# Kernel optimization log

Measured on AMD Instinct MI355X. Metric: run time of the kernel, lower is better.

Reference implementation:

```python
import jax, jax.numpy as jnp
import numpy as np

NUM_HEADS = 8
WINDOW_SIZE = 4
DIM = 384


def setup_inputs() -> dict:
    key = jax.random.key(0)
    k_x, k_qkv, k_pw, k_pb = jax.random.split(key, 4)
    B, N, C = 8, 16384, DIM
    x = jax.random.normal(k_x, (B, N, C), dtype=jnp.float32)
    # torch nn.Linear weights are [out_features, in_features]
    W_qkv = jax.random.normal(k_qkv, (3 * C, C), dtype=jnp.float32) * (1.0 / np.sqrt(C))
    W_proj = jax.random.normal(k_pw, (C, C), dtype=jnp.float32) * (1.0 / np.sqrt(C))
    b_proj = jax.random.normal(k_pb, (C,), dtype=jnp.float32) * 0.01
    return {"x": x, "W_qkv": W_qkv, "W_proj": W_proj, "b_proj": b_proj}


def reference(x, W_qkv, W_proj, b_proj):
    B, N, C = x.shape
    H = int(round(N ** 0.5))
    W = H
    ws = WINDOW_SIZE
    nh = NUM_HEADS
    hd = C // nh
    scale = hd ** -0.5
    hw, ww = H // ws, W // ws

    qkv = x @ W_qkv.T  # [B, N, 3C]
    qkv = qkv.reshape(B, N, 3, nh, hd)
    qkv = jnp.transpose(qkv, (2, 0, 3, 1, 4))  # [3, B, nh, N, hd]
    q, k, v = qkv[0], qkv[1], qkv[2]

    def to_windows(t):
        # [B, nh, N, hd] -> [B, nh, n_windows, ws*ws, hd]
        t = t.reshape(B, nh, hw, ws, ww, ws, hd)
        t = jnp.transpose(t, (0, 1, 2, 4, 3, 5, 6))
        return t.reshape(B, nh, hw * ww, ws * ws, hd)

    q, k, v = to_windows(q), to_windows(k), to_windows(v)

    attn = jnp.einsum('bhwqd,bhwkd->bhwqk', q, k) * scale
    attn = jax.nn.softmax(attn, axis=-1)
    out = jnp.einsum('bhwqk,bhwkd->bhwqd', attn, v)

    # windows back to [B, N, C]
    out = out.reshape(B, nh, hw, ww, ws, ws, hd)
    out = jnp.transpose(out, (0, 1, 2, 4, 3, 5, 6)).reshape(B, nh, N, hd)
    out = jnp.transpose(out, (0, 2, 1, 3)).reshape(B, N, C)

    out = out @ W_proj.T + b_proj
    return out
```

## Files before the change

### kernel.cpp

```cpp
#include <hip/hip_runtime.h>
#include <hip/hip_bf16.h>
#include <cstdint>

#define ASPACE(n) __attribute__((address_space(n)))

typedef short bf16x8 __attribute__((ext_vector_type(8)));
typedef float f32x4 __attribute__((ext_vector_type(4)));

__device__ __forceinline__ unsigned short f2bf(float f) {
  uint32_t u = __float_as_uint(f);
  u += 0x7fffu + ((u >> 16) & 1u);
  return (unsigned short)(u >> 16);
}
__device__ __forceinline__ float bf2f(unsigned short h) {
  return __uint_as_float(((uint32_t)h) << 16);
}

__global__ __launch_bounds__(256) void conv_f32_bf16(const float4* __restrict__ src,
                                                     ushort4* __restrict__ dst, int n4) {
  int i = blockIdx.x * blockDim.x + threadIdx.x;
  int stride = gridDim.x * blockDim.x;
  for (; i < n4; i += stride) {
    float4 v = src[i];
    ushort4 o;
    o.x = f2bf(v.x); o.y = f2bf(v.y); o.z = f2bf(v.z); o.w = f2bf(v.w);
    dst[i] = o;
  }
}


__device__ __forceinline__ void gload16(const unsigned short* g, unsigned short* l) {
  __builtin_amdgcn_global_load_lds((const ASPACE(1) void*)g, (ASPACE(3) void*)l, 16, 0, 0);
}

template <int OUT_MODE>
__global__ __launch_bounds__(256, 3) void gemm_bt(const unsigned short* __restrict__ A,
                                                  const unsigned short* __restrict__ B,
                                                  void* __restrict__ Cout,
                                                  const float* __restrict__ bias,
                                                  int M, int N, int K) {
  __shared__ unsigned short As[2][128 * 32];
  __shared__ unsigned short Bs[2][192 * 32];

  const int tid  = threadIdx.x;
  const int lane = tid & 63;
  const int wave = tid >> 6;
  const int wr = wave >> 1;
  const int wc = wave & 1;

  const int nwg = gridDim.x;
  const int swz = (blockIdx.x & 7) * (nwg >> 3) + (blockIdx.x >> 3);
  const int ntn = N / 192;
  const int bn0 = (swz % ntn) * 192;
  const int bm0 = (swz / ntn) << 7;

  const unsigned short* Abase = A + (size_t)bm0 * K;
  const unsigned short* Bbase = B + (size_t)bn0 * K;

  const unsigned short* gA[2];
  const unsigned short* gB[3];
  unsigned short* lA[2];
  unsigned short* lB[3];
#pragma unroll
  for (int i = 0; i < 2; ++i) {
    const int c = i * 256 + tid;
    const int r = c >> 2;
    const int gc = (c & 3) ^ ((r >> 1) & 3);
    gA[i] = Abase + (size_t)r * K + gc * 8;
    lA[i] = (unsigned short*)As + (i * 256 + wave * 64) * 8;
  }
#pragma unroll
  for (int i = 0; i < 3; ++i) {
    const int c = i * 256 + tid;
    const int r = c >> 2;
    const int gc = (c & 3) ^ ((r >> 1) & 3);
    gB[i] = Bbase + (size_t)r * K + gc * 8;
    lB[i] = (unsigned short*)Bs + (i * 256 + wave * 64) * 8;
  }
  const int abufoff = 128 * 32;
  const int bbufoff = 192 * 32;

  const int fr = lane & 15;
  const int hi = lane >> 4;
  int afo[4], bfo[6];
#pragma unroll
  for (int m = 0; m < 4; ++m) {
    const int row = wr * 64 + m * 16 + fr;
    afo[m] = row * 32 + ((hi ^ ((row >> 1) & 3)) * 8);
  }
#pragma unroll
  for (int n = 0; n < 6; ++n) {
    const int row = wc * 96 + n * 16 + fr;
    bfo[n] = row * 32 + ((hi ^ ((row >> 1) & 3)) * 8);
  }

  f32x4 acc[4][6];
#pragma unroll
  for (int m = 0; m < 4; ++m)
#pragma unroll
    for (int n = 0; n < 6; ++n) {
      f32x4 z = {0.f, 0.f, 0.f, 0.f};
      acc[m][n] = z;
    }

  const int NT = K >> 5;

#pragma unroll
  for (int i = 0; i < 2; ++i) gload16(gA[i], lA[i]);
#pragma unroll
  for (int i = 0; i < 3; ++i) gload16(gB[i], lB[i]);
  __syncthreads();

  int cur = 0;
  for (int t = 0; t < NT; ++t) {
    if (t + 1 < NT) {
      const int nb = cur ^ 1;
      const int k0 = (t + 1) << 5;
#pragma unroll
      for (int i = 0; i < 2; ++i) gload16(gA[i] + k0, lA[i] + nb * abufoff);
#pragma unroll
      for (int i = 0; i < 3; ++i) gload16(gB[i] + k0, lB[i] + nb * bbufoff);
    }
    {
      const unsigned short* Ab = (const unsigned short*)As + cur * abufoff;
      const unsigned short* Bb = (const unsigned short*)Bs + cur * bbufoff;
      bf16x8 af[4], bfv[6];
#pragma unroll
      for (int m = 0; m < 4; ++m) af[m] = *(const bf16x8*)(Ab + afo[m]);
#pragma unroll
      for (int n = 0; n < 6; ++n) bfv[n] = *(const bf16x8*)(Bb + bfo[n]);
#pragma unroll
      for (int m = 0; m < 4; ++m)
#pragma unroll
        for (int n = 0; n < 6; ++n)
          acc[m][n] = __builtin_amdgcn_mfma_f32_16x16x32_bf16(af[m], bfv[n], acc[m][n], 0, 0, 0);
    }
    __syncthreads();
    cur ^= 1;
  }

  const int rq = hi * 4;
  if (OUT_MODE == 1) {
    float* C = (float*)Cout;
#pragma unroll
    for (int m = 0; m < 4; ++m) {
#pragma unroll
      for (int n = 0; n < 6; ++n) {
        const int col = bn0 + wc * 96 + n * 16 + fr;
        const float bv = bias[col];
#pragma unroll
        for (int r = 0; r < 4; ++r) {
          const int row = bm0 + wr * 64 + m * 16 + rq + r;
          C[(size_t)row * N + col] = acc[m][n][r] + bv;
        }
      }
    }
  } else {
    unsigned short* C = (unsigned short*)Cout;
#pragma unroll
    for (int m = 0; m < 4; ++m) {
#pragma unroll
      for (int n = 0; n < 6; ++n) {
        const int col = bn0 + wc * 96 + n * 16 + fr;
#pragma unroll
        for (int r = 0; r < 4; ++r) {
          const int row = bm0 + wr * 64 + m * 16 + rq + r;
          C[(size_t)row * N + col] = f2bf(acc[m][n][r]);
        }
      }
    }
  }
}

#define PADV 24
#define PADP 24
__global__ __launch_bounds__(256) void win_attn(const unsigned short* __restrict__ qkv,
                                                unsigned short* __restrict__ aout) {
  __shared__ unsigned short lds[4][48 * PADV + 16 * PADP];
  const int tid = threadIdx.x;
  const int wave = tid >> 6, lane = tid & 63;
  const int wg = blockIdx.x * 4 + wave;
  const int h = wg & 7;
  const int bw = wg >> 3;
  const int w = bw & 1023, b = bw >> 10;
  const int wy = w >> 5, wx = w & 31;

  unsigned short* Vt = lds[wave];
  unsigned short* P  = lds[wave] + 48 * PADV;

  const int lg = lane >> 4;
  const int lr = lane & 15;

  const int n_lr = (wy * 4 + (lr >> 2)) * 128 + wx * 4 + (lr & 3);
  const size_t rowbase = ((size_t)(b * 16384 + n_lr)) * 1152 + h * 48;

  bf16x8 aq0, bk0;
  bf16x8 aq1 = {0, 0, 0, 0, 0, 0, 0, 0};
  bf16x8 bk1 = {0, 0, 0, 0, 0, 0, 0, 0};
  aq0 = *(const bf16x8*)(qkv + rowbase + lg * 8);
  bk0 = *(const bf16x8*)(qkv + rowbase + 384 + lg * 8);
  if (lg < 2) {
    aq1 = *(const bf16x8*)(qkv + rowbase + 32 + lg * 8);
    bk1 = *(const bf16x8*)(qkv + rowbase + 384 + 32 + lg * 8);
  }

  {
    bf16x8 v = *(const bf16x8*)(qkv + rowbase + 768 + lg * 8);
#pragma unroll
    for (int i = 0; i < 8; ++i) Vt[(lg * 8 + i) * PADV + lr] = (unsigned short)v[i];
    if (lane < 32) {
      bf16x8 v2 = *(const bf16x8*)(qkv + rowbase + 768 + 32 + lg * 8);
#pragma unroll
      for (int i = 0; i < 8; ++i) Vt[((4 + lg) * 8 + i) * PADV + lr] = (unsigned short)v2[i];
    }
  }

  f32x4 s = {0.f, 0.f, 0.f, 0.f};
  s = __builtin_amdgcn_mfma_f32_16x16x32_bf16(aq0, bk0, s, 0, 0, 0);
  s = __builtin_amdgcn_mfma_f32_16x16x32_bf16(aq1, bk1, s, 0, 0, 0);

  const float scale = 0.14433756729740643f;
  float p[4];
#pragma unroll
  for (int r = 0; r < 4; ++r) {
    float x = s[r] * scale;
    float m = x;
    m = fmaxf(m, __shfl_xor(m, 1));
    m = fmaxf(m, __shfl_xor(m, 2));
    m = fmaxf(m, __shfl_xor(m, 4));
    m = fmaxf(m, __shfl_xor(m, 8));
    float e = __expf(x - m);
    float t = e;
    t += __shfl_xor(t, 1);
    t += __shfl_xor(t, 2);
    t += __shfl_xor(t, 4);
    t += __shfl_xor(t, 8);
    p[r] = e / t;
  }
#pragma unroll
  for (int r = 0; r < 4; ++r) P[(lg * 4 + r) * PADP + lr] = f2bf(p[r]);

  __syncthreads();

  bf16x8 ap = {0, 0, 0, 0, 0, 0, 0, 0};
  if (lg < 2) ap = *(const bf16x8*)(P + lr * PADP + lg * 8);

  f32x4 o[3];
#pragma unroll
  for (int c = 0; c < 3; ++c) {
    bf16x8 bv = {0, 0, 0, 0, 0, 0, 0, 0};
    if (lg < 2) bv = *(const bf16x8*)(Vt + (c * 16 + lr) * PADV + lg * 8);
    f32x4 z = {0.f, 0.f, 0.f, 0.f};
    o[c] = __builtin_amdgcn_mfma_f32_16x16x32_bf16(ap, bv, z, 0, 0, 0);
  }

#pragma unroll
  for (int r = 0; r < 4; ++r) {
    const int qi = lg * 4 + r;
    const int nq = (wy * 4 + (qi >> 2)) * 128 + wx * 4 + (qi & 3);
    const size_t obase = ((size_t)(b * 16384 + nq)) * 384 + h * 48;
#pragma unroll
    for (int c = 0; c < 3; ++c)
      aout[obase + c * 16 + lr] = f2bf(o[c][r]);
  }
}

extern "C" void kernel_launch(void* const* d_in, const int* in_sizes, int n_in,
                              void* d_out, int out_size, void* d_ws, size_t ws_size,
                              hipStream_t stream) {
  const float* x      = (const float*)d_in[0];
  const float* W_qkv  = (const float*)d_in[1];
  const float* W_proj = (const float*)d_in[2];
  const float* b_proj = (const float*)d_in[3];
  float* out = (float*)d_out;

  const int Bb = 8, Nn = 16384, Cc = 384;
  const int M = Bb * Nn;
  const int threeC = 3 * Cc;

  char* ws = (char*)d_ws;
  unsigned short* qkv_bf  = (unsigned short*)ws;
  unsigned short* xa_bf   = (unsigned short*)(ws + (size_t)M * threeC * 2);
  unsigned short* wqkv_bf = (unsigned short*)(ws + (size_t)M * threeC * 2 + (size_t)M * Cc * 2);
  unsigned short* wproj_bf = wqkv_bf + threeC * Cc;

  conv_f32_bf16<<<2048, 256, 0, stream>>>((const float4*)x, (ushort4*)xa_bf, M * Cc / 4);
  conv_f32_bf16<<<432, 256, 0, stream>>>((const float4*)W_qkv, (ushort4*)wqkv_bf, threeC * Cc / 4);
  conv_f32_bf16<<<144, 256, 0, stream>>>((const float4*)W_proj, (ushort4*)wproj_bf, Cc * Cc / 4);

  gemm_bt<0><<<(M / 128) * (threeC / 192), 256, 0, stream>>>(xa_bf, wqkv_bf, qkv_bf, nullptr,
                                                             M, threeC, Cc);

  win_attn<<<Bb * 8 * 1024 / 4, 256, 0, stream>>>(qkv_bf, xa_bf);

  gemm_bt<1><<<(M / 128) * (Cc / 192), 256, 0, stream>>>(xa_bf, wproj_bf, out, b_proj,
                                                         M, Cc, Cc);
}
```

Before: 417.8 us.

## Fuse QKV projection with window attention, reading fp32 input directly

Replaces the separate x-to-bf16 conversion, the QKV GEMM and the window-attention kernel with one kernel. Each workgroup computes the Q, K and V columns for one head over a 4x32 token strip and keeps them in LDS. It then runs the window attention from LDS, so the large bf16 QKV buffer is never written to or read back from global memory. The fp32 input is converted to bf16 in registers with packed cvt instructions. The cost is that each x tile is loaded once per head, eight times in total, and the swizzle is meant to keep those reuses within one L2. It also uses more LDS and runs at lower occupancy.

```diff
diff --git a/kernel.cpp b/kernel.cpp
--- a/kernel.cpp
+++ b/kernel.cpp
@@ -14,6 +14,15 @@
 }
 __device__ __forceinline__ float bf2f(unsigned short h) {
   return __uint_as_float(((uint32_t)h) << 16);
+}
+
+__device__ __forceinline__ bf16x8 cvt8(float4 a, float4 b) {
+  union { uint32_t u[4]; bf16x8 v; } r;
+  asm("v_cvt_pk_bf16_f32 %0, %1, %2" : "=v"(r.u[0]) : "v"(a.x), "v"(a.y));
+  asm("v_cvt_pk_bf16_f32 %0, %1, %2" : "=v"(r.u[1]) : "v"(a.z), "v"(a.w));
+  asm("v_cvt_pk_bf16_f32 %0, %1, %2" : "=v"(r.u[2]) : "v"(b.x), "v"(b.y));
+  asm("v_cvt_pk_bf16_f32 %0, %1, %2" : "=v"(r.u[3]) : "v"(b.z), "v"(b.w));
+  return r.v;
 }
 
 __global__ __launch_bounds__(256) void conv_f32_bf16(const float4* __restrict__ src,
@@ -28,9 +37,190 @@
   }
 }
 
-
 __device__ __forceinline__ void gload16(const unsigned short* g, unsigned short* l) {
   __builtin_amdgcn_global_load_lds((const ASPACE(1) void*)g, (ASPACE(3) void*)l, 16, 0, 0);
+}
+
+__global__ __launch_bounds__(256, 2) void fused_qkv_attn(const float* __restrict__ x,
+                                                         const unsigned short* __restrict__ Wq,
+                                                         unsigned short* __restrict__ aout) {
+  __shared__ unsigned short lds[9216 + 18432];
+  unsigned short* Bs  = lds;
+  unsigned short* qkv = lds + 9216;
+  unsigned short* scratch = lds;
+
+  const int tid = threadIdx.x, lane = tid & 63, wave = tid >> 6;
+  const int nwg = gridDim.x;
+  const int swz = (blockIdx.x & 7) * (nwg >> 3) + (blockIdx.x >> 3);
+  const int h  = swz & 7;
+  const int tg = swz >> 3;
+  const int b = tg >> 7, yb = (tg >> 2) & 31, xb = tg & 3;
+  const int tokbase = b * 16384 + (yb * 4) * 128 + xb * 32;
+
+  const int c0 = tid,        r0 = c0 >> 2;
+  const int c1 = 256 + tid,  r1 = c1 >> 2;
+  const int c2 = 512 + lane, r2 = c2 >> 2;
+  const int gc0 = (c0 & 3) ^ ((r0 >> 1) & 3);
+  const int gc1 = (c1 & 3) ^ ((r1 >> 1) & 3);
+  const int gc2 = (c2 & 3) ^ ((r2 >> 1) & 3);
+  const unsigned short* gB0 = Wq + (size_t)((r0 / 48) * 384 + h * 48 + (r0 % 48)) * 384 + gc0 * 8;
+  const unsigned short* gB1 = Wq + (size_t)((r1 / 48) * 384 + h * 48 + (r1 % 48)) * 384 + gc1 * 8;
+  const unsigned short* gB2 = Wq + (size_t)((r2 / 48) * 384 + h * 48 + (r2 % 48)) * 384 + gc2 * 8;
+  unsigned short* lB0 = Bs + (0 * 256 + wave * 64) * 8;
+  unsigned short* lB1 = Bs + (1 * 256 + wave * 64) * 8;
+  unsigned short* lB2 = Bs + 512 * 8;
+
+  const int fr = lane & 15;
+  const int hi = lane >> 4;
+
+  int bfo[9];
+#pragma unroll
+  for (int n = 0; n < 9; ++n) {
+    const int row = n * 16 + fr;
+    bfo[n] = row * 32 + ((hi ^ ((row >> 1) & 3)) * 8);
+  }
+
+  const float* pA0 = x + (size_t)(tokbase + wave * 128 + fr) * 384 + hi * 8;
+  const float* pA1 = pA0 + (size_t)16 * 384;
+
+  f32x4 acc[2][9];
+#pragma unroll
+  for (int mf = 0; mf < 2; ++mf)
+#pragma unroll
+    for (int n = 0; n < 9; ++n) {
+      f32x4 z = {0.f, 0.f, 0.f, 0.f};
+      acc[mf][n] = z;
+    }
+
+  gload16(gB0, lB0); gload16(gB1, lB1);
+  if (wave == 0) gload16(gB2, lB2);
+  float4 a00 = *(const float4*)(pA0);
+  float4 a01 = *(const float4*)(pA0 + 4);
+  float4 a10 = *(const float4*)(pA1);
+  float4 a11 = *(const float4*)(pA1 + 4);
+  __syncthreads();
+
+#pragma unroll
+  for (int t = 0; t < 12; ++t) {
+    const int buf = t & 1;
+    if (t < 11) {
+      const int k0 = (t + 1) * 32;
+      const int nb = (t + 1) & 1;
+      gload16(gB0 + k0, lB0 + nb * 4608);
+      gload16(gB1 + k0, lB1 + nb * 4608);
+      if (wave == 0) gload16(gB2 + k0, lB2 + nb * 4608);
+    }
+    bf16x8 af0 = cvt8(a00, a01);
+    bf16x8 af1 = cvt8(a10, a11);
+    if (t < 11) {
+      const int ko = (t + 1) * 32;
+      a00 = *(const float4*)(pA0 + ko);
+      a01 = *(const float4*)(pA0 + ko + 4);
+      a10 = *(const float4*)(pA1 + ko);
+      a11 = *(const float4*)(pA1 + ko + 4);
+    }
+    const unsigned short* Bb = Bs + buf * 4608;
+    bf16x8 bfv[9];
+#pragma unroll
+    for (int n = 0; n < 9; ++n) bfv[n] = *(const bf16x8*)(Bb + bfo[n]);
+#pragma unroll
+    for (int n = 0; n < 9; ++n) {
+      acc[0][n] = __builtin_amdgcn_mfma_f32_16x16x32_bf16(af0, bfv[n], acc[0][n], 0, 0, 0);
+      acc[1][n] = __builtin_amdgcn_mfma_f32_16x16x32_bf16(af1, bfv[n], acc[1][n], 0, 0, 0);
+    }
+    __syncthreads();
+  }
+
+  {
+    unsigned short* qb = qkv + (32 * wave + hi * 4) * 144 + fr;
+#pragma unroll
+    for (int mf = 0; mf < 2; ++mf)
+#pragma unroll
+      for (int n = 0; n < 9; ++n)
+#pragma unroll
+        for (int r = 0; r < 4; ++r)
+          qb[(16 * mf + r) * 144 + n * 16] = f2bf(acc[mf][n][r]);
+  }
+  __syncthreads();
+
+  unsigned short* Vt = scratch + wave * 1536;
+  unsigned short* P  = Vt + 48 * 24;
+  const int lg = hi;
+  const int lr = fr;
+
+  for (int wi = 0; wi < 2; ++wi) {
+    const int wxl = wave * 2 + wi;
+    const int btok = (lr >> 2) * 32 + wxl * 4 + (lr & 3);
+    const unsigned short* qrow = qkv + btok * 144;
+
+    bf16x8 aq0 = *(const bf16x8*)(qrow + lg * 8);
+    bf16x8 bk0 = *(const bf16x8*)(qrow + 48 + lg * 8);
+    bf16x8 aq1 = {0, 0, 0, 0, 0, 0, 0, 0};
+    bf16x8 bk1 = {0, 0, 0, 0, 0, 0, 0, 0};
+    if (lg < 2) {
+      aq1 = *(const bf16x8*)(qrow + 32 + lg * 8);
+      bk1 = *(const bf16x8*)(qrow + 80 + lg * 8);
+    }
+    {
+      bf16x8 v = *(const bf16x8*)(qrow + 96 + lg * 8);
+#pragma unroll
+      for (int i = 0; i < 8; ++i) Vt[(lg * 8 + i) * 24 + lr] = (unsigned short)v[i];
+      if (lane < 32) {
+        bf16x8 v2 = *(const bf16x8*)(qrow + 128 + lg * 8);
+#pragma unroll
+        for (int i = 0; i < 8; ++i) Vt[((4 + lg) * 8 + i) * 24 + lr] = (unsigned short)v2[i];
+      }
+    }
+
+    f32x4 s = {0.f, 0.f, 0.f, 0.f};
+    s = __builtin_amdgcn_mfma_f32_16x16x32_bf16(aq0, bk0, s, 0, 0, 0);
+    s = __builtin_amdgcn_mfma_f32_16x16x32_bf16(aq1, bk1, s, 0, 0, 0);
+
+    const float scale = 0.14433756729740643f;
+    float p[4];
+#pragma unroll
+    for (int r = 0; r < 4; ++r) {
+      float xv = s[r] * scale;
+      float m = xv;
+      m = fmaxf(m, __shfl_xor(m, 1));
+      m = fmaxf(m, __shfl_xor(m, 2));
+      m = fmaxf(m, __shfl_xor(m, 4));
+      m = fmaxf(m, __shfl_xor(m, 8));
+      float e = __expf(xv - m);
+      float tt = e;
+      tt += __shfl_xor(tt, 1);
+      tt += __shfl_xor(tt, 2);
+      tt += __shfl_xor(tt, 4);
+      tt += __shfl_xor(tt, 8);
+      p[r] = e / tt;
+    }
+#pragma unroll
+    for (int r = 0; r < 4; ++r) P[(lg * 4 + r) * 24 + lr] = f2bf(p[r]);
+
+    __syncthreads();
+
+    bf16x8 ap = {0, 0, 0, 0, 0, 0, 0, 0};
+    if (lg < 2) ap = *(const bf16x8*)(P + lr * 24 + lg * 8);
+
+    f32x4 o[3];
+#pragma unroll
+    for (int c = 0; c < 3; ++c) {
+      bf16x8 bv = {0, 0, 0, 0, 0, 0, 0, 0};
+      if (lg < 2) bv = *(const bf16x8*)(Vt + (c * 16 + lr) * 24 + lg * 8);
+      f32x4 z = {0.f, 0.f, 0.f, 0.f};
+      o[c] = __builtin_amdgcn_mfma_f32_16x16x32_bf16(ap, bv, z, 0, 0, 0);
+    }
+
+#pragma unroll
+    for (int r = 0; r < 4; ++r) {
+      const int qi = lg * 4 + r;
+      const int g = tokbase + (qi >> 2) * 128 + wxl * 4 + (qi & 3);
+      unsigned short* ob = aout + (size_t)g * 384 + h * 48;
+#pragma unroll
+      for (int c = 0; c < 3; ++c) ob[c * 16 + lr] = f2bf(o[c][r]);
+    }
+    __syncthreads();
+  }
 }
 
 template <int OUT_MODE>
@@ -172,99 +362,6 @@
   }
 }
 
-#define PADV 24
-#define PADP 24
-__global__ __launch_bounds__(256) void win_attn(const unsigned short* __restrict__ qkv,
-                                                unsigned short* __restrict__ aout) {
-  __shared__ unsigned short lds[4][48 * PADV + 16 * PADP];
-  const int tid = threadIdx.x;
-  const int wave = tid >> 6, lane = tid & 63;
-  const int wg = blockIdx.x * 4 + wave;
-  const int h = wg & 7;
-  const int bw = wg >> 3;
-  const int w = bw & 1023, b = bw >> 10;
-  const int wy = w >> 5, wx = w & 31;
-
-  unsigned short* Vt = lds[wave];
-  unsigned short* P  = lds[wave] + 48 * PADV;
-
-  const int lg = lane >> 4;
-  const int lr = lane & 15;
-
-  const int n_lr = (wy * 4 + (lr >> 2)) * 128 + wx * 4 + (lr & 3);
-  const size_t rowbase = ((size_t)(b * 16384 + n_lr)) * 1152 + h * 48;
-
-  bf16x8 aq0, bk0;
-  bf16x8 aq1 = {0, 0, 0, 0, 0, 0, 0, 0};
-  bf16x8 bk1 = {0, 0, 0, 0, 0, 0, 0, 0};
-  aq0 = *(const bf16x8*)(qkv + rowbase + lg * 8);
-  bk0 = *(const bf16x8*)(qkv + rowbase + 384 + lg * 8);
-  if (lg < 2) {
-    aq1 = *(const bf16x8*)(qkv + rowbase + 32 + lg * 8);
-    bk1 = *(const bf16x8*)(qkv + rowbase + 384 + 32 + lg * 8);
-  }
-
-  {
-    bf16x8 v = *(const bf16x8*)(qkv + rowbase + 768 + lg * 8);
-#pragma unroll
-    for (int i = 0; i < 8; ++i) Vt[(lg * 8 + i) * PADV + lr] = (unsigned short)v[i];
-    if (lane < 32) {
-      bf16x8 v2 = *(const bf16x8*)(qkv + rowbase + 768 + 32 + lg * 8);
-#pragma unroll
-      for (int i = 0; i < 8; ++i) Vt[((4 + lg) * 8 + i) * PADV + lr] = (unsigned short)v2[i];
-    }
-  }
-
-  f32x4 s = {0.f, 0.f, 0.f, 0.f};
-  s = __builtin_amdgcn_mfma_f32_16x16x32_bf16(aq0, bk0, s, 0, 0, 0);
-  s = __builtin_amdgcn_mfma_f32_16x16x32_bf16(aq1, bk1, s, 0, 0, 0);
-
-  const float scale = 0.14433756729740643f;
-  float p[4];
-#pragma unroll
-  for (int r = 0; r < 4; ++r) {
-    float x = s[r] * scale;
-    float m = x;
-    m = fmaxf(m, __shfl_xor(m, 1));
-    m = fmaxf(m, __shfl_xor(m, 2));
-    m = fmaxf(m, __shfl_xor(m, 4));
-    m = fmaxf(m, __shfl_xor(m, 8));
-    float e = __expf(x - m);
-    float t = e;
-    t += __shfl_xor(t, 1);
-    t += __shfl_xor(t, 2);
-    t += __shfl_xor(t, 4);
-    t += __shfl_xor(t, 8);
-    p[r] = e / t;
-  }
-#pragma unroll
-  for (int r = 0; r < 4; ++r) P[(lg * 4 + r) * PADP + lr] = f2bf(p[r]);
-
-  __syncthreads();
-
-  bf16x8 ap = {0, 0, 0, 0, 0, 0, 0, 0};
-  if (lg < 2) ap = *(const bf16x8*)(P + lr * PADP + lg * 8);
-
-  f32x4 o[3];
-#pragma unroll
-  for (int c = 0; c < 3; ++c) {
-    bf16x8 bv = {0, 0, 0, 0, 0, 0, 0, 0};
-    if (lg < 2) bv = *(const bf16x8*)(Vt + (c * 16 + lr) * PADV + lg * 8);
-    f32x4 z = {0.f, 0.f, 0.f, 0.f};
-    o[c] = __builtin_amdgcn_mfma_f32_16x16x32_bf16(ap, bv, z, 0, 0, 0);
-  }
-
-#pragma unroll
-  for (int r = 0; r < 4; ++r) {
-    const int qi = lg * 4 + r;
-    const int nq = (wy * 4 + (qi >> 2)) * 128 + wx * 4 + (qi & 3);
-    const size_t obase = ((size_t)(b * 16384 + nq)) * 384 + h * 48;
-#pragma unroll
-    for (int c = 0; c < 3; ++c)
-      aout[obase + c * 16 + lr] = f2bf(o[c][r]);
-  }
-}
-
 extern "C" void kernel_launch(void* const* d_in, const int* in_sizes, int n_in,
                               void* d_out, int out_size, void* d_ws, size_t ws_size,
                               hipStream_t stream) {
@@ -279,19 +376,16 @@
   const int threeC = 3 * Cc;
 
   char* ws = (char*)d_ws;
-  unsigned short* qkv_bf  = (unsigned short*)ws;
-  unsigned short* xa_bf   = (unsigned short*)(ws + (size_t)M * threeC * 2);
-  unsigned short* wqkv_bf = (unsigned short*)(ws + (size_t)M * threeC * 2 + (size_t)M * Cc * 2);
+  unsigned short* xa_bf    = (unsigned short*)ws;
+  unsigned short* wqkv_bf  = (unsigned short*)(ws + (size_t)M * Cc * 2);
   unsigned short* wproj_bf = wqkv_bf + threeC * Cc;
 
-  conv_f32_bf16<<<2048, 256, 0, stream>>>((const float4*)x, (ushort4*)xa_bf, M * Cc / 4);
-  conv_f32_bf16<<<432, 256, 0, stream>>>((const float4*)W_qkv, (ushort4*)wqkv_bf, threeC * Cc / 4);
-  conv_f32_bf16<<<144, 256, 0, stream>>>((const float4*)W_proj, (ushort4*)wproj_bf, Cc * Cc / 4);
-
-  gemm_bt<0><<<(M / 128) * (threeC / 192), 256, 0, stream>>>(xa_bf, wqkv_bf, qkv_bf, nullptr,
-                                                             M, threeC, Cc);
-
-  win_attn<<<Bb * 8 * 1024 / 4, 256, 0, stream>>>(qkv_bf, xa_bf);
+  conv_f32_bf16<<<432, 256, 0, stream>>>((const float4*)W_qkv, (ushort4*)wqkv_bf,
+                                         threeC * Cc / 4);
+  conv_f32_bf16<<<144, 256, 0, stream>>>((const float4*)W_proj, (ushort4*)wproj_bf,
+                                         Cc * Cc / 4);
+
+  fused_qkv_attn<<<8192, 256, 0, stream>>>(x, wqkv_bf, xa_bf);
 
   gemm_bt<1><<<(M / 128) * (Cc / 192), 256, 0, stream>>>(xa_bf, wproj_bf, out, b_proj,
                                                          M, Cc, Cc);
```

Result: slower. 430.7 us (+3.1%).

## Fuse fp32-to-bf16 conversion of x into the QKV GEMM operand load

Applied to the files above, without the earlier changes.

Removes the separate pass that converts x from fp32 to bf16 and adds a QKV GEMM variant that streams fp32 x tiles into LDS and converts them to bf16 in registers with packed convert instructions before the MFMA. This saves a full read of x plus a write and re-read of its bf16 copy. In exchange, the A tile in LDS doubles in size and occupancy hint drops to 2, and because the GEMM grid reads x once per N tile, it reads more fp32 bytes from global memory than the bf16 version did.

```diff
diff --git a/kernel.cpp b/kernel.cpp
--- a/kernel.cpp
+++ b/kernel.cpp
@@ -14,6 +14,15 @@
 }
 __device__ __forceinline__ float bf2f(unsigned short h) {
   return __uint_as_float(((uint32_t)h) << 16);
+}
+
+__device__ __forceinline__ bf16x8 cvt8(float4 a, float4 b) {
+  union { uint32_t u[4]; bf16x8 v; } r;
+  asm("v_cvt_pk_bf16_f32 %0, %1, %2" : "=v"(r.u[0]) : "v"(a.x), "v"(a.y));
+  asm("v_cvt_pk_bf16_f32 %0, %1, %2" : "=v"(r.u[1]) : "v"(a.z), "v"(a.w));
+  asm("v_cvt_pk_bf16_f32 %0, %1, %2" : "=v"(r.u[2]) : "v"(b.x), "v"(b.y));
+  asm("v_cvt_pk_bf16_f32 %0, %1, %2" : "=v"(r.u[3]) : "v"(b.z), "v"(b.w));
+  return r.v;
 }
 
 __global__ __launch_bounds__(256) void conv_f32_bf16(const float4* __restrict__ src,
@@ -28,9 +37,135 @@
   }
 }
 
-
 __device__ __forceinline__ void gload16(const unsigned short* g, unsigned short* l) {
   __builtin_amdgcn_global_load_lds((const ASPACE(1) void*)g, (ASPACE(3) void*)l, 16, 0, 0);
+}
+__device__ __forceinline__ void gload16f(const float* g, float* l) {
+  __builtin_amdgcn_global_load_lds((const ASPACE(1) void*)g, (ASPACE(3) void*)l, 16, 0, 0);
+}
+
+__global__ __launch_bounds__(256, 2) void gemm_qkv_xf32(const float* __restrict__ A,
+                                                        const unsigned short* __restrict__ B,
+                                                        unsigned short* __restrict__ C,
+                                                        int M, int N, int K) {
+  __shared__ float Asf[2][128 * 32];
+  __shared__ unsigned short Bs[2][192 * 32];
+
+  const int tid  = threadIdx.x;
+  const int lane = tid & 63;
+  const int wave = tid >> 6;
+  const int wr = wave >> 1;
+  const int wc = wave & 1;
+
+  const int nwg = gridDim.x;
+  const int swz = (blockIdx.x & 7) * (nwg >> 3) + (blockIdx.x >> 3);
+  const int ntn = N / 192;
+  const int bn0 = (swz % ntn) * 192;
+  const int bm0 = (swz / ntn) << 7;
+
+  const float* Abase = A + (size_t)bm0 * K;
+  const unsigned short* Bbase = B + (size_t)bn0 * K;
+
+  const float* gA[4];
+  float* lA[4];
+#pragma unroll
+  for (int i = 0; i < 4; ++i) {
+    const int c = i * 256 + tid;
+    const int r = c >> 3;
+    const int gc = (c & 7) ^ (r & 7);
+    gA[i] = Abase + (size_t)r * K + gc * 4;
+    lA[i] = (float*)Asf + (i * 256 + wave * 64) * 4;
+  }
+  const unsigned short* gB[3];
+  unsigned short* lB[3];
+#pragma unroll
+  for (int i = 0; i < 3; ++i) {
+    const int c = i * 256 + tid;
+    const int r = c >> 2;
+    const int gc = (c & 3) ^ ((r >> 1) & 3);
+    gB[i] = Bbase + (size_t)r * K + gc * 8;
+    lB[i] = (unsigned short*)Bs + (i * 256 + wave * 64) * 8;
+  }
+  const int abufoff = 128 * 32;
+  const int bbufoff = 192 * 32;
+
+  const int fr = lane & 15;
+  const int hi = lane >> 4;
+  int afo[4];
+#pragma unroll
+  for (int m = 0; m < 4; ++m) {
+    const int row = wr * 64 + m * 16 + fr;
+    afo[m] = row * 32 + (((2 * hi) ^ (row & 7)) * 4);
+  }
+  int bfo[6];
+#pragma unroll
+  for (int n = 0; n < 6; ++n) {
+    const int row = wc * 96 + n * 16 + fr;
+    bfo[n] = row * 32 + ((hi ^ ((row >> 1) & 3)) * 8);
+  }
+
+  f32x4 acc[4][6];
+#pragma unroll
+  for (int m = 0; m < 4; ++m)
+#pragma unroll
+    for (int n = 0; n < 6; ++n) {
+      f32x4 z = {0.f, 0.f, 0.f, 0.f};
+      acc[m][n] = z;
+    }
+
+  const int NT = K >> 5;
+
+#pragma unroll
+  for (int i = 0; i < 4; ++i) gload16f(gA[i], lA[i]);
+#pragma unroll
+  for (int i = 0; i < 3; ++i) gload16(gB[i], lB[i]);
+  __syncthreads();
+
+  int cur = 0;
+  for (int t = 0; t < NT; ++t) {
+    if (t + 1 < NT) {
+      const int nb = cur ^ 1;
+      const int k0 = (t + 1) << 5;
+#pragma unroll
+      for (int i = 0; i < 4; ++i) gload16f(gA[i] + k0, lA[i] + nb * abufoff);
+#pragma unroll
+      for (int i = 0; i < 3; ++i) gload16(gB[i] + k0, lB[i] + nb * bbufoff);
+    }
+    {
+      const float* Af = (const float*)Asf + cur * abufoff;
+      const unsigned short* Bb = (const unsigned short*)Bs + cur * bbufoff;
+      bf16x8 af[4], bfv[6];
+#pragma unroll
+      for (int m = 0; m < 4; ++m) {
+        float4 lo = *(const float4*)(Af + afo[m]);
+        float4 hi4 = *(const float4*)(Af + (afo[m] ^ 4));
+        af[m] = cvt8(lo, hi4);
+      }
+#pragma unroll
+      for (int n = 0; n < 6; ++n) bfv[n] = *(const bf16x8*)(Bb + bfo[n]);
+#pragma unroll
+      for (int m = 0; m < 4; ++m)
+#pragma unroll
+        for (int n = 0; n < 6; ++n)
+          acc[m][n] = __builtin_amdgcn_mfma_f32_16x16x32_bf16(af[m], bfv[n], acc[m][n], 0, 0, 0);
+    }
+    __syncthreads();
+    cur ^= 1;
+  }
+
+  const int rq = hi * 4;
+#pragma unroll
+  for (int m = 0; m < 4; ++m) {
+#pragma unroll
+    for (int n = 0; n < 6; ++n) {
+      const int col = bn0 + wc * 96 + n * 16 + fr;
+#pragma unroll
+      for (int r = 0; r < 4; ++r) {
+        const int row = bm0 + wr * 64 + m * 16 + rq + r;
+        C[(size_t)row * N + col] = f2bf(acc[m][n][r]);
+      }
+    }
+  }
 }
 
 template <int OUT_MODE>
@@ -279,17 +414,18 @@
   const int threeC = 3 * Cc;
 
   char* ws = (char*)d_ws;
-  unsigned short* qkv_bf  = (unsigned short*)ws;
-  unsigned short* xa_bf   = (unsigned short*)(ws + (size_t)M * threeC * 2);
-  unsigned short* wqkv_bf = (unsigned short*)(ws + (size_t)M * threeC * 2 + (size_t)M * Cc * 2);
+  unsigned short* qkv_bf   = (unsigned short*)ws;
+  unsigned short* xa_bf    = (unsigned short*)(ws + (size_t)M * threeC * 2);
+  unsigned short* wqkv_bf  = (unsigned short*)(ws + (size_t)M * threeC * 2 + (size_t)M * Cc * 2);
   unsigned short* wproj_bf = wqkv_bf + threeC * Cc;
 
-  conv_f32_bf16<<<2048, 256, 0, stream>>>((const float4*)x, (ushort4*)xa_bf, M * Cc / 4);
-  conv_f32_bf16<<<432, 256, 0, stream>>>((const float4*)W_qkv, (ushort4*)wqkv_bf, threeC * Cc / 4);
-  conv_f32_bf16<<<144, 256, 0, stream>>>((const float4*)W_proj, (ushort4*)wproj_bf, Cc * Cc / 4);
-
-  gemm_bt<0><<<(M / 128) * (threeC / 192), 256, 0, stream>>>(xa_bf, wqkv_bf, qkv_bf, nullptr,
-                                                             M, threeC, Cc);
+  conv_f32_bf16<<<432, 256, 0, stream>>>((const float4*)W_qkv, (ushort4*)wqkv_bf,
+                                         threeC * Cc / 4);
+  conv_f32_bf16<<<144, 256, 0, stream>>>((const float4*)W_proj, (ushort4*)wproj_bf,
+                                         Cc * Cc / 4);
+
+  gemm_qkv_xf32<<<(M / 128) * (threeC / 192), 256, 0, stream>>>(x, wqkv_bf, qkv_bf,
+                                                                M, threeC, Cc);
 
   win_attn<<<Bb * 8 * 1024 / 4, 256, 0, stream>>>(qkv_bf, xa_bf);
 
```

Result: slower. 436.5 us (+4.5%).
